# Kernel tuning notes

Measured on AMD Instinct MI355X. Metric: run time of the kernel, lower is better.

The kernel has to match this reference:

```python
import jax, jax.numpy as jnp
import numpy as np

N = 16384          # num nodes (128 graphs x 128 turbines)
E = 262144         # edges before self loops
TURBINE_NUM = 128
D_IN = 512         # input_dim (= 2*hidden_dim1)
H1 = 256           # hidden_dim1
H2 = 256           # hidden_dim2
NEG_SLOPE = 0.2    # PyG GATConv default leaky relu slope


def _glorot(key, shape, fan_in):
    return jax.random.normal(key, shape, dtype=jnp.float32) / np.sqrt(fan_in)


def setup_inputs() -> dict:
    key = jax.random.key(0)
    ks = jax.random.split(key, 12)
    x = jax.random.normal(ks[0], (N, H2), dtype=jnp.float32)
    adj = jax.random.randint(ks[1], (2, E), 0, N, dtype=jnp.int64)
    # fc: Linear(hidden_dim2 -> hidden_dim1); stored as [in, out]
    W_fc = _glorot(ks[2], (H2, H1), H2)
    b_fc = jnp.zeros((H1,), dtype=jnp.float32)
    # gat1: GATConv(H1 -> H1, heads=2, concat)
    W1 = _glorot(ks[3], (H1, 2 * H1), H1)
    a1_src = _glorot(ks[4], (2, H1), H1)
    a1_dst = _glorot(ks[5], (2, H1), H1)
    b1 = jnp.zeros((2 * H1,), dtype=jnp.float32)
    # gat2: GATConv(D_IN -> D_IN, heads=1, concat)
    W2 = _glorot(ks[6], (D_IN, D_IN), D_IN)
    a2_src = _glorot(ks[7], (1, D_IN), D_IN)
    a2_dst = _glorot(ks[8], (1, D_IN), D_IN)
    b2 = jnp.zeros((D_IN,), dtype=jnp.float32)
    return dict(x=x, adj=adj, W_fc=W_fc, b_fc=b_fc, W1=W1, a1_src=a1_src,
                a1_dst=a1_dst, b1=b1, W2=W2, a2_src=a2_src, a2_dst=a2_dst, b2=b2)


def gat_conv(x, src, dst, W, a_src, a_dst, bias, heads, out_ch):
    """PyG GATConv (eval mode, self loops already in src/dst)."""
    n = x.shape[0]
    h = (x @ W).reshape(n, heads, out_ch)                 # [N,H,C]
    al_s = jnp.einsum('nhc,hc->nh', h, a_src)             # [N,H]
    al_d = jnp.einsum('nhc,hc->nh', h, a_dst)
    e = jax.nn.leaky_relu(al_s[src] + al_d[dst], NEG_SLOPE)  # [E,H]
    # segment softmax over incoming edges per destination node
    e_max = jax.ops.segment_max(e, dst, num_segments=n)
    e_exp = jnp.exp(e - e_max[dst])
    denom = jax.ops.segment_sum(e_exp, dst, num_segments=n)
    alpha = e_exp / (denom[dst] + 1e-16)                  # [E,H]
    msg = h[src] * alpha[:, :, None]                      # [E,H,C]
    out = jax.ops.segment_sum(msg, dst, num_segments=n)   # [N,H,C]
    return out.reshape(n, heads * out_ch) + bias


def reference(x, adj, W_fc, b_fc, W1, a1_src, a1_dst, b1, W2, a2_src, a2_dst, b2):
    # add self loops (PyG GATConv default)
    loops = jnp.arange(N, dtype=adj.dtype)
    src = jnp.concatenate([adj[0], loops])
    dst = jnp.concatenate([adj[1], loops])
    h = jax.nn.relu(x @ W_fc + b_fc)                      # fc + ReLU
    h = gat_conv(h, src, dst, W1, a1_src, a1_dst, b1, heads=2, out_ch=H1)
    h = jax.nn.relu(h)
    h = gat_conv(h, src, dst, W2, a2_src, a2_dst, b2, heads=1, out_ch=D_IN)
    y = jax.nn.relu(h)
    return y.reshape(-1, TURBINE_NUM, y.shape[1])         # [128,128,512]
```

## Files before the change

### kernel.cpp

```cpp
#include <hip/hip_runtime.h>

#define N_NODES 16384
#define N_EDGES 262144
#define E_TOT   (N_EDGES + N_NODES)
#define NEG_SLOPE 0.2f
#define SLOTS 64

typedef __attribute__((ext_vector_type(8))) short short8;
typedef __attribute__((ext_vector_type(4))) float floatx4;
typedef __attribute__((ext_vector_type(4))) int intx4;

__device__ __forceinline__ float bf2f(ushort u) {
    return __uint_as_float(((unsigned)u) << 16);
}
__device__ __forceinline__ ushort f2bf(float f) {
    unsigned u = __float_as_uint(f);
    u += 0x7fffu + ((u >> 16) & 1u);
    return (ushort)(u >> 16);
}
__device__ __forceinline__ float leaky(float x) {
    return x > 0.f ? x : NEG_SLOPE * x;
}

#define PREP_T1     65536
#define PREP_T2     (PREP_T1 + 131072)
#define PREP_Z      (PREP_T2 + 262144)
#define PREP_ZA     (PREP_Z + 4096)
#define PREP_V      (PREP_ZA + 24576)
#define PREP_TOT    (PREP_V + 131072)

__global__ __launch_bounds__(256) void k_prep(const float* __restrict__ Wfc,
                                              ushort* __restrict__ WfcT,
                                              const float* __restrict__ W1,
                                              ushort* __restrict__ W1T,
                                              const float* __restrict__ W2,
                                              ushort* __restrict__ W2T,
                                              int* __restrict__ counts,
                                              int* __restrict__ alzero,
                                              const float* __restrict__ a1s,
                                              const float* __restrict__ a1d,
                                              const float* __restrict__ a2s,
                                              const float* __restrict__ a2d,
                                              float* __restrict__ v1s,
                                              float* __restrict__ v1d,
                                              float* __restrict__ v2s,
                                              float* __restrict__ v2d) {
    int idx = blockIdx.x * 256 + threadIdx.x;
    if (idx < PREP_T1) {
        int t = idx;
        int k = t >> 8, n = t & 255;
        WfcT[n * 256 + k] = f2bf(Wfc[t]);
    } else if (idx < PREP_T2) {
        int t = idx - PREP_T1;
        int k = t >> 9, n = t & 511;
        W1T[n * 256 + k] = f2bf(W1[t]);
    } else if (idx < PREP_Z) {
        int t = idx - PREP_T2;
        int k = t >> 9, n = t & 511;
        W2T[n * 512 + k] = f2bf(W2[t]);
    } else if (idx < PREP_ZA) {
        int t = idx - PREP_Z;
        *(intx4*)(counts + t * 4) = (intx4){0, 0, 0, 0};
    } else if (idx < PREP_V) {
        int t = idx - PREP_ZA;
        *(intx4*)(alzero + t * 4) = (intx4){0, 0, 0, 0};
    } else if (idx < PREP_TOT) {
        int t = idx - PREP_V;
        int w = t >> 6, lane = t & 63;
        int grp = w >> 9;
        int o = w & 511;
        float sum;
        if (grp < 2) {
            const float* a = grp ? a1d : a1s;
            int h = o >> 8, k = o & 255;
            const float* wr = W1 + (size_t)k * 512 + h * 256;
            const float* ar = a + h * 256;
            floatx4 wv = *(const floatx4*)(wr + lane * 4);
            floatx4 av = *(const floatx4*)(ar + lane * 4);
            sum = wv[0]*av[0] + wv[1]*av[1] + wv[2]*av[2] + wv[3]*av[3];
        } else {
            const float* a = (grp == 2) ? a2s : a2d;
            const float* wr = W2 + (size_t)o * 512;
            floatx4 w0 = *(const floatx4*)(wr + lane * 8);
            floatx4 w1 = *(const floatx4*)(wr + lane * 8 + 4);
            floatx4 a0 = *(const floatx4*)(a + lane * 8);
            floatx4 a1 = *(const floatx4*)(a + lane * 8 + 4);
            sum = w0[0]*a0[0] + w0[1]*a0[1] + w0[2]*a0[2] + w0[3]*a0[3]
                + w1[0]*a1[0] + w1[1]*a1[1] + w1[2]*a1[2] + w1[3]*a1[3];
        }
#pragma unroll
        for (int msk = 1; msk < 64; msk <<= 1) sum += __shfl_xor(sum, msk, 64);
        if (lane == 0) {
            float* dst = (grp == 0) ? v1s : (grp == 1) ? v1d
                        : (grp == 2) ? v2s : v2d;
            dst[o] = sum;
        }
    }
}

__global__ __launch_bounds__(256) void k_scatter(const int* __restrict__ adj,
                                                 int* __restrict__ counts,
                                                 int* __restrict__ esrc) {
    int e = blockIdx.x * 256 + threadIdx.x;
    if (e < E_TOT) {
        int s, d;
        if (e < N_EDGES) { s = adj[e]; d = adj[N_EDGES + e]; }
        else             { s = e - N_EDGES; d = s; }
        int pos = atomicAdd(&counts[d], 1);
        esrc[(d << 6) + pos] = s;
    }
}

#define GM 128
#define GN 128
#define GK 64
#define LDK2 72

__global__ __launch_bounds__(256) void gemm128(const void* __restrict__ Av,
                                               int a_f32, int lda, int agrp,
                                               const ushort* __restrict__ BT,
                                               const float* __restrict__ bias,
                                               ushort* __restrict__ C,
                                               float* __restrict__ Cf,
                                               int Nc, int K, int relu,
                                               const float* __restrict__ vs,
                                               const float* __restrict__ vd,
                                               float* __restrict__ als,
                                               float* __restrict__ ald,
                                               int heads) {
    __shared__ ushort As[GM * LDK2];
    __shared__ ushort Bs[GN * LDK2];
    int tid = threadIdx.x, wave = tid >> 6, lane = tid & 63;
    int quad = lane >> 4, l16 = lane & 15;
    int bm = blockIdx.x * GM, bn = blockIdx.y * GN;
    int wm = (wave & 1) * 64, wn = (wave >> 1) * 64;
    int abase = (bn >> 8) * agrp;

    const ushort* Ab = (const ushort*)Av;
    const float*  Af = (const float*)Av;

    floatx4 acc[4][4];
#pragma unroll
    for (int mi = 0; mi < 4; mi++)
#pragma unroll
        for (int ni = 0; ni < 4; ni++)
            acc[mi][ni] = (floatx4){0.f, 0.f, 0.f, 0.f};

    int srow[4], scol[4];
#pragma unroll
    for (int t = 0; t < 4; t++) {
        int ci = tid + 256 * t;
        srow[t] = ci >> 3;
        scol[t] = (ci & 7) * 8;
    }

    short8 av[4], bv[4];
    floatx4 fa0[4], fa1[4];

    if (a_f32) {
#pragma unroll
        for (int t = 0; t < 4; t++) {
            const float* pa = Af + (size_t)(bm + srow[t]) * lda + abase + scol[t];
            fa0[t] = *(const floatx4*)pa;
            fa1[t] = *(const floatx4*)(pa + 4);
        }
    } else {
#pragma unroll
        for (int t = 0; t < 4; t++)
            av[t] = *(const short8*)(Ab + (size_t)(bm + srow[t]) * lda + abase + scol[t]);
    }
#pragma unroll
    for (int t = 0; t < 4; t++)
        bv[t] = *(const short8*)(BT + (size_t)(bn + srow[t]) * K + scol[t]);

    for (int kb = 0; kb < K; kb += GK) {
        if (kb) {
            asm volatile("s_waitcnt lgkmcnt(0)" ::: "memory");
            __builtin_amdgcn_sched_barrier(0);
            __builtin_amdgcn_s_barrier();
            __builtin_amdgcn_sched_barrier(0);
        }
        if (a_f32) {
#pragma unroll
            for (int t = 0; t < 4; t++) {
                short8 r;
                r[0] = (short)f2bf(fa0[t][0]); r[1] = (short)f2bf(fa0[t][1]);
                r[2] = (short)f2bf(fa0[t][2]); r[3] = (short)f2bf(fa0[t][3]);
                r[4] = (short)f2bf(fa1[t][0]); r[5] = (short)f2bf(fa1[t][1]);
                r[6] = (short)f2bf(fa1[t][2]); r[7] = (short)f2bf(fa1[t][3]);
                *(short8*)&As[srow[t] * LDK2 + scol[t]] = r;
            }
        } else {
#pragma unroll
            for (int t = 0; t < 4; t++)
                *(short8*)&As[srow[t] * LDK2 + scol[t]] = av[t];
        }
#pragma unroll
        for (int t = 0; t < 4; t++)
            *(short8*)&Bs[srow[t] * LDK2 + scol[t]] = bv[t];
        asm volatile("s_waitcnt lgkmcnt(0)" ::: "memory");
        __builtin_amdgcn_sched_barrier(0);
        __builtin_amdgcn_s_barrier();
        __builtin_amdgcn_sched_barrier(0);

        if (kb + GK < K) {
            if (a_f32) {
#pragma unroll
                for (int t = 0; t < 4; t++) {
                    const float* pa = Af + (size_t)(bm + srow[t]) * lda + abase + kb + GK + scol[t];
                    fa0[t] = *(const floatx4*)pa;
                    fa1[t] = *(const floatx4*)(pa + 4);
                }
            } else {
#pragma unroll
                for (int t = 0; t < 4; t++)
                    av[t] = *(const short8*)(Ab + (size_t)(bm + srow[t]) * lda + abase + kb + GK + scol[t]);
            }
#pragma unroll
            for (int t = 0; t < 4; t++)
                bv[t] = *(const short8*)(BT + (size_t)(bn + srow[t]) * K + kb + GK + scol[t]);
            __builtin_amdgcn_sched_barrier(0);
        }

#pragma unroll
        for (int kk = 0; kk < GK; kk += 32) {
            short8 af[4], bf[4];
#pragma unroll
            for (int mi = 0; mi < 4; mi++)
                af[mi] = *(const short8*)&As[(wm + mi * 16 + l16) * LDK2 + kk + quad * 8];
#pragma unroll
            for (int ni = 0; ni < 4; ni++)
                bf[ni] = *(const short8*)&Bs[(wn + ni * 16 + l16) * LDK2 + kk + quad * 8];
#pragma unroll
            for (int mi = 0; mi < 4; mi++)
#pragma unroll
                for (int ni = 0; ni < 4; ni++)
                    acc[mi][ni] = __builtin_amdgcn_mfma_f32_16x16x32_bf16(
                        af[mi], bf[ni], acc[mi][ni], 0, 0, 0);
        }
    }

#pragma unroll
    for (int mi = 0; mi < 4; mi++) {
        int row = bm + wm + mi * 16 + quad * 4;
#pragma unroll
        for (int ni = 0; ni < 4; ni++) {
            int col = bn + wn + ni * 16 + l16;
            float bv2 = bias ? bias[col] : 0.f;
#pragma unroll
            for (int i = 0; i < 4; i++) {
                float v = acc[mi][ni][i] + bv2;
                if (relu) v = fmaxf(v, 0.f);
                acc[mi][ni][i] = v;
                if (Cf) Cf[(size_t)(row + i) * Nc + col] = v;
                else    C[(size_t)(row + i) * Nc + col] = f2bf(v);
            }
        }
    }

    if (als) {
        if (heads == 2) {
            float s0[4], s1[4], d0[4], d1[4];
#pragma unroll
            for (int ni = 0; ni < 4; ni++) {
                int col = bn + wn + ni * 16 + l16;
                s0[ni] = vs[col];  s1[ni] = vs[256 + col];
                d0[ni] = vd[col];  d1[ni] = vd[256 + col];
            }
#pragma unroll
            for (int mi = 0; mi < 4; mi++) {
#pragma unroll
                for (int i = 0; i < 4; i++) {
                    float aS0 = 0.f, aS1 = 0.f, aD0 = 0.f, aD1 = 0.f;
#pragma unroll
                    for (int ni = 0; ni < 4; ni++) {
                        float vv = acc[mi][ni][i];
                        aS0 += vv * s0[ni]; aS1 += vv * s1[ni];
                        aD0 += vv * d0[ni]; aD1 += vv * d1[ni];
                    }
#pragma unroll
                    for (int msk = 1; msk < 16; msk <<= 1) {
                        aS0 += __shfl_xor(aS0, msk, 64);
                        aS1 += __shfl_xor(aS1, msk, 64);
                        aD0 += __shfl_xor(aD0, msk, 64);
                        aD1 += __shfl_xor(aD1, msk, 64);
                    }
                    if (l16 == 0) {
                        int row = bm + wm + mi * 16 + quad * 4 + i;
                        atomicAdd(&als[row * 2],     aS0);
                        atomicAdd(&als[row * 2 + 1], aS1);
                        atomicAdd(&ald[row * 2],     aD0);
                        atomicAdd(&ald[row * 2 + 1], aD1);
                    }
                }
            }
        } else {
            float aS[4], aD[4];
#pragma unroll
            for (int ni = 0; ni < 4; ni++) {
                int col = bn + wn + ni * 16 + l16;
                aS[ni] = vs[col];
                aD[ni] = vd[col];
            }
#pragma unroll
            for (int mi = 0; mi < 4; mi++) {
#pragma unroll
                for (int i = 0; i < 4; i++) {
                    float dS = 0.f, dD = 0.f;
#pragma unroll
                    for (int ni = 0; ni < 4; ni++) {
                        dS += acc[mi][ni][i] * aS[ni];
                        dD += acc[mi][ni][i] * aD[ni];
                    }
#pragma unroll
                    for (int msk = 1; msk < 16; msk <<= 1) {
                        dS += __shfl_xor(dS, msk, 64);
                        dD += __shfl_xor(dD, msk, 64);
                    }
                    if (l16 == 0) {
                        int row = bm + wm + mi * 16 + quad * 4 + i;
                        atomicAdd(&als[row], dS);
                        atomicAdd(&ald[row], dD);
                    }
                }
            }
        }
    }
}

__global__ __launch_bounds__(256) void k_agg(const ushort* __restrict__ h,
                                             const float* __restrict__ als,
                                             const float* __restrict__ ald,
                                             const int* __restrict__ counts,
                                             const int* __restrict__ esrc,
                                             ushort* __restrict__ outb,
                                             int heads) {
    int wave = threadIdx.x >> 6, lane = threadIdx.x & 63;
    int n = blockIdx.x * 4 + wave;
    int base = n << 6;
    int deg  = counts[n];

    int myhead = (heads == 2) ? (lane >> 5) : 0;
    int cs = (heads == 2) ? ((lane & 31) * 8) : (lane * 8);
    int stride = (heads == 2) ? 256 : 512;

    float aldh0 = ald[n * heads];
    float aldh1 = (heads == 2) ? ald[n * heads + 1] : 0.f;
    const ushort* hc = h + cs;

    float acc[8];
#pragma unroll
    for (int q = 0; q < 8; q++) acc[q] = 0.f;
    float ws0 = 0.f, ws1 = 0.f;

    for (int cb = 0; cb < deg; cb += 64) {
        int i = cb + lane;
        int sv = 0;
        float w0 = 0.f, w1 = 0.f;
        if (i < deg) {
            sv = esrc[base + i];
            w0 = __expf(leaky(als[sv * heads] + aldh0));
            if (heads == 2) w1 = __expf(leaky(als[sv * 2 + 1] + aldh1));
            ws0 += w0; ws1 += w1;
        }
        int cnt = min(64, deg - cb);
        int j = 0;
        for (; j + 4 <= cnt; j += 4) {
            int sj0 = __shfl(sv, j, 64);
            int sj1 = __shfl(sv, j + 1, 64);
            int sj2 = __shfl(sv, j + 2, 64);
            int sj3 = __shfl(sv, j + 3, 64);
            float a00 = __shfl(w0, j, 64),     a01 = __shfl(w1, j, 64);
            float a10 = __shfl(w0, j + 1, 64), a11 = __shfl(w1, j + 1, 64);
            float a20 = __shfl(w0, j + 2, 64), a21 = __shfl(w1, j + 2, 64);
            float a30 = __shfl(w0, j + 3, 64), a31 = __shfl(w1, j + 3, 64);
            float al0 = myhead ? a01 : a00;
            float al1 = myhead ? a11 : a10;
            float al2 = myhead ? a21 : a20;
            float al3 = myhead ? a31 : a30;
            short8 h0v = *(const short8*)(hc + (size_t)sj0 * stride);
            short8 h1v = *(const short8*)(hc + (size_t)sj1 * stride);
            short8 h2v = *(const short8*)(hc + (size_t)sj2 * stride);
            short8 h3v = *(const short8*)(hc + (size_t)sj3 * stride);
#pragma unroll
            for (int q = 0; q < 8; q++) {
                acc[q] += al0 * bf2f((ushort)h0v[q]);
                acc[q] += al1 * bf2f((ushort)h1v[q]);
                acc[q] += al2 * bf2f((ushort)h2v[q]);
                acc[q] += al3 * bf2f((ushort)h3v[q]);
            }
        }
        for (; j < cnt; j++) {
            int s = __shfl(sv, j, 64);
            float a0 = __shfl(w0, j, 64), a1 = __shfl(w1, j, 64);
            float al = myhead ? a1 : a0;
            short8 hv = *(const short8*)(hc + (size_t)s * stride);
#pragma unroll
            for (int q = 0; q < 8; q++) acc[q] += al * bf2f((ushort)hv[q]);
        }
    }

#pragma unroll
    for (int msk = 1; msk < 64; msk <<= 1) {
        ws0 += __shfl_xor(ws0, msk, 64);
        ws1 += __shfl_xor(ws1, msk, 64);
    }
    float inv = 1.f / ((myhead ? ws1 : ws0) + 1e-16f);

    short8 r;
#pragma unroll
    for (int q = 0; q < 8; q++) r[q] = (short)f2bf(acc[q] * inv);
    *(short8*)(outb + (size_t)n * 512 + lane * 8) = r;
}

extern "C" void kernel_launch(void* const* d_in, const int* in_sizes, int n_in,
                              void* d_out, int out_size, void* d_ws, size_t ws_size,
                              hipStream_t stream) {
    const float* x   = (const float*)d_in[0];
    const int*   adj = (const int*)d_in[1];
    const float* Wfc = (const float*)d_in[2];
    const float* bfc = (const float*)d_in[3];
    const float* W1  = (const float*)d_in[4];
    const float* a1s = (const float*)d_in[5];
    const float* a1d = (const float*)d_in[6];
    const float* b1  = (const float*)d_in[7];
    const float* W2  = (const float*)d_in[8];
    const float* a2s = (const float*)d_in[9];
    const float* a2d = (const float*)d_in[10];
    const float* b2  = (const float*)d_in[11];
    float* out = (float*)d_out;

    char* ws = (char*)d_ws;
    size_t off = 0;
    auto alloc = [&](size_t bytes) -> void* {
        void* p = ws + off;
        off += (bytes + 255) & ~(size_t)255;
        return p;
    };
    ushort* h0b  = (ushort*)alloc((size_t)N_NODES * 256 * 2);
    ushort* hub  = (ushort*)alloc((size_t)N_NODES * 512 * 2);
    ushort* g1b  = (ushort*)alloc((size_t)N_NODES * 512 * 2);
    int* counts  = (int*)alloc(N_NODES * 4);
    int* esrc    = (int*)alloc((size_t)N_NODES * SLOTS * 4);
    ushort* WfcT = (ushort*)alloc(256 * 256 * 2);
    ushort* W1T  = (ushort*)alloc(512 * 256 * 2);
    ushort* W2T  = (ushort*)alloc(512 * 512 * 2);
    float* als1  = (float*)alloc(N_NODES * 2 * 4);
    float* ald1  = (float*)alloc(N_NODES * 2 * 4);
    float* als2  = (float*)alloc(N_NODES * 4);
    float* ald2  = (float*)alloc(N_NODES * 4);
    float* v1s   = (float*)alloc(512 * 4);
    float* v1d   = (float*)alloc(512 * 4);
    float* v2s   = (float*)alloc(512 * 4);
    float* v2d   = (float*)alloc(512 * 4);

    k_prep<<<PREP_TOT / 256, 256, 0, stream>>>(Wfc, WfcT, W1, W1T, W2, W2T,
                                               counts, (int*)als1,
                                               a1s, a1d, a2s, a2d,
                                               v1s, v1d, v2s, v2d);

    k_scatter<<<(E_TOT + 255) / 256, 256, 0, stream>>>(adj, counts, esrc);

    gemm128<<<dim3(N_NODES / GM, 256 / GN), 256, 0, stream>>>(
        x, 1, 256, 0, WfcT, bfc, h0b, nullptr, 256, 256, 1,
        v1s, v1d, als1, ald1, 2);
    k_agg<<<N_NODES / 4, 256, 0, stream>>>(h0b, als1, ald1, counts, esrc, hub, 2);

    gemm128<<<dim3(N_NODES / GM, 512 / GN), 256, 0, stream>>>(
        hub, 0, 512, 256, W1T, b1, g1b, nullptr, 512, 256, 1,
        v2s, v2d, als2, ald2, 1);
    k_agg<<<N_NODES / 4, 256, 0, stream>>>(g1b, als2, ald2, counts, esrc, hub, 1);

    gemm128<<<dim3(N_NODES / GM, 512 / GN), 256, 0, stream>>>(
        hub, 0, 512, 0, W2T, b2, nullptr, out, 512, 512, 1,
        nullptr, nullptr, nullptr, nullptr, 0);
}
```

Measured before the change: 220.7 us.

## Split GEMM into LDS fp32-input kernel and direct-register bf16 GEMM without shared memory

The generic GEMM is split into two kernels. One is a specialized LDS-staged kernel for the first fp32-input layer with compile-time dimensions. The other, a new gemm_direct used for the bf16 layers, loads MFMA fragments straight from global memory into registers with double-buffered prefetch, skipping the LDS stage and its barriers. This removes LDS writes and sync overhead, but each wave now reads A and B tiles redundantly from global/L2 (no sharing across waves), and the loads are short strided 16-byte rows that may coalesce less well.

```diff
diff --git a/kernel.cpp b/kernel.cpp
--- a/kernel.cpp
+++ b/kernel.cpp
@@ -116,28 +116,21 @@
 #define GK 64
 #define LDK2 72
 
-__global__ __launch_bounds__(256) void gemm128(const void* __restrict__ Av,
-                                               int a_f32, int lda, int agrp,
-                                               const ushort* __restrict__ BT,
-                                               const float* __restrict__ bias,
-                                               ushort* __restrict__ C,
-                                               float* __restrict__ Cf,
-                                               int Nc, int K, int relu,
-                                               const float* __restrict__ vs,
-                                               const float* __restrict__ vd,
-                                               float* __restrict__ als,
-                                               float* __restrict__ ald,
-                                               int heads) {
+__global__ __launch_bounds__(256) void gemm1_lds(const float* __restrict__ Af,
+                                                 const ushort* __restrict__ BT,
+                                                 const float* __restrict__ bias,
+                                                 ushort* __restrict__ C,
+                                                 const float* __restrict__ vs,
+                                                 const float* __restrict__ vd,
+                                                 float* __restrict__ als,
+                                                 float* __restrict__ ald) {
     __shared__ ushort As[GM * LDK2];
     __shared__ ushort Bs[GN * LDK2];
+    const int lda = 256, K = 256, Nc = 256;
     int tid = threadIdx.x, wave = tid >> 6, lane = tid & 63;
     int quad = lane >> 4, l16 = lane & 15;
     int bm = blockIdx.x * GM, bn = blockIdx.y * GN;
     int wm = (wave & 1) * 64, wn = (wave >> 1) * 64;
-    int abase = (bn >> 8) * agrp;
-
-    const ushort* Ab = (const ushort*)Av;
-    const float*  Af = (const float*)Av;
 
     floatx4 acc[4][4];
 #pragma unroll
@@ -154,24 +147,15 @@
         scol[t] = (ci & 7) * 8;
     }
 
-    short8 av[4], bv[4];
+    short8 bv[4];
     floatx4 fa0[4], fa1[4];
-
-    if (a_f32) {
-#pragma unroll
-        for (int t = 0; t < 4; t++) {
-            const float* pa = Af + (size_t)(bm + srow[t]) * lda + abase + scol[t];
-            fa0[t] = *(const floatx4*)pa;
-            fa1[t] = *(const floatx4*)(pa + 4);
-        }
-    } else {
-#pragma unroll
-        for (int t = 0; t < 4; t++)
-            av[t] = *(const short8*)(Ab + (size_t)(bm + srow[t]) * lda + abase + scol[t]);
-    }
-#pragma unroll
-    for (int t = 0; t < 4; t++)
+#pragma unroll
+    for (int t = 0; t < 4; t++) {
+        const float* pa = Af + (size_t)(bm + srow[t]) * lda + scol[t];
+        fa0[t] = *(const floatx4*)pa;
+        fa1[t] = *(const floatx4*)(pa + 4);
         bv[t] = *(const short8*)(BT + (size_t)(bn + srow[t]) * K + scol[t]);
+    }
 
     for (int kb = 0; kb < K; kb += GK) {
         if (kb) {
@@ -180,45 +164,29 @@
             __builtin_amdgcn_s_barrier();
             __builtin_amdgcn_sched_barrier(0);
         }
-        if (a_f32) {
-#pragma unroll
-            for (int t = 0; t < 4; t++) {
-                short8 r;
-                r[0] = (short)f2bf(fa0[t][0]); r[1] = (short)f2bf(fa0[t][1]);
-                r[2] = (short)f2bf(fa0[t][2]); r[3] = (short)f2bf(fa0[t][3]);
-                r[4] = (short)f2bf(fa1[t][0]); r[5] = (short)f2bf(fa1[t][1]);
-                r[6] = (short)f2bf(fa1[t][2]); r[7] = (short)f2bf(fa1[t][3]);
-                *(short8*)&As[srow[t] * LDK2 + scol[t]] = r;
-            }
-        } else {
-#pragma unroll
-            for (int t = 0; t < 4; t++)
-                *(short8*)&As[srow[t] * LDK2 + scol[t]] = av[t];
-        }
-#pragma unroll
-        for (int t = 0; t < 4; t++)
+#pragma unroll
+        for (int t = 0; t < 4; t++) {
+            short8 r;
+            r[0] = (short)f2bf(fa0[t][0]); r[1] = (short)f2bf(fa0[t][1]);
+            r[2] = (short)f2bf(fa0[t][2]); r[3] = (short)f2bf(fa0[t][3]);
+            r[4] = (short)f2bf(fa1[t][0]); r[5] = (short)f2bf(fa1[t][1]);
+            r[6] = (short)f2bf(fa1[t][2]); r[7] = (short)f2bf(fa1[t][3]);
+            *(short8*)&As[srow[t] * LDK2 + scol[t]] = r;
             *(short8*)&Bs[srow[t] * LDK2 + scol[t]] = bv[t];
+        }
         asm volatile("s_waitcnt lgkmcnt(0)" ::: "memory");
         __builtin_amdgcn_sched_barrier(0);
         __builtin_amdgcn_s_barrier();
         __builtin_amdgcn_sched_barrier(0);
 
         if (kb + GK < K) {
-            if (a_f32) {
-#pragma unroll
-                for (int t = 0; t < 4; t++) {
-                    const float* pa = Af + (size_t)(bm + srow[t]) * lda + abase + kb + GK + scol[t];
-                    fa0[t] = *(const floatx4*)pa;
-                    fa1[t] = *(const floatx4*)(pa + 4);
-                }
-            } else {
-#pragma unroll
-                for (int t = 0; t < 4; t++)
-                    av[t] = *(const short8*)(Ab + (size_t)(bm + srow[t]) * lda + abase + kb + GK + scol[t]);
-            }
-#pragma unroll
-            for (int t = 0; t < 4; t++)
+#pragma unroll
+            for (int t = 0; t < 4; t++) {
+                const float* pa = Af + (size_t)(bm + srow[t]) * lda + kb + GK + scol[t];
+                fa0[t] = *(const floatx4*)pa;
+                fa1[t] = *(const floatx4*)(pa + 4);
                 bv[t] = *(const short8*)(BT + (size_t)(bn + srow[t]) * K + kb + GK + scol[t]);
+            }
             __builtin_amdgcn_sched_barrier(0);
         }
 
@@ -237,6 +205,128 @@
                 for (int ni = 0; ni < 4; ni++)
                     acc[mi][ni] = __builtin_amdgcn_mfma_f32_16x16x32_bf16(
                         af[mi], bf[ni], acc[mi][ni], 0, 0, 0);
+        }
+    }
+
+#pragma unroll
+    for (int mi = 0; mi < 4; mi++) {
+        int row = bm + wm + mi * 16 + quad * 4;
+#pragma unroll
+        for (int ni = 0; ni < 4; ni++) {
+            int col = bn + wn + ni * 16 + l16;
+            float bv2 = bias[col];
+#pragma unroll
+            for (int i = 0; i < 4; i++) {
+                float v = fmaxf(acc[mi][ni][i] + bv2, 0.f);
+                acc[mi][ni][i] = v;
+                C[(size_t)(row + i) * Nc + col] = f2bf(v);
+            }
+        }
+    }
+
+    float s0[4], s1[4], d0[4], d1[4];
+#pragma unroll
+    for (int ni = 0; ni < 4; ni++) {
+        int col = bn + wn + ni * 16 + l16;
+        s0[ni] = vs[col];  s1[ni] = vs[256 + col];
+        d0[ni] = vd[col];  d1[ni] = vd[256 + col];
+    }
+#pragma unroll
+    for (int mi = 0; mi < 4; mi++) {
+#pragma unroll
+        for (int i = 0; i < 4; i++) {
+            float aS0 = 0.f, aS1 = 0.f, aD0 = 0.f, aD1 = 0.f;
+#pragma unroll
+            for (int ni = 0; ni < 4; ni++) {
+                float vv = acc[mi][ni][i];
+                aS0 += vv * s0[ni]; aS1 += vv * s1[ni];
+                aD0 += vv * d0[ni]; aD1 += vv * d1[ni];
+            }
+#pragma unroll
+            for (int msk = 1; msk < 16; msk <<= 1) {
+                aS0 += __shfl_xor(aS0, msk, 64);
+                aS1 += __shfl_xor(aS1, msk, 64);
+                aD0 += __shfl_xor(aD0, msk, 64);
+                aD1 += __shfl_xor(aD1, msk, 64);
+            }
+            if (l16 == 0) {
+                int row = bm + wm + mi * 16 + quad * 4 + i;
+                atomicAdd(&als[row * 2],     aS0);
+                atomicAdd(&als[row * 2 + 1], aS1);
+                atomicAdd(&ald[row * 2],     aD0);
+                atomicAdd(&ald[row * 2 + 1], aD1);
+            }
+        }
+    }
+}
+
+__global__ __launch_bounds__(256) void gemm_direct(const ushort* __restrict__ A,
+                                                   int lda, int agrp,
+                                                   const ushort* __restrict__ BT,
+                                                   const float* __restrict__ bias,
+                                                   ushort* __restrict__ C,
+                                                   float* __restrict__ Cf,
+                                                   int Nc, int K, int relu,
+                                                   const float* __restrict__ vs,
+                                                   const float* __restrict__ vd,
+                                                   float* __restrict__ als,
+                                                   float* __restrict__ ald) {
+    int tid = threadIdx.x, wave = tid >> 6, lane = tid & 63;
+    int quad = lane >> 4, l16 = lane & 15;
+    int bm = blockIdx.x * GM, bn = blockIdx.y * GN;
+    int wm = (wave & 1) * 64, wn = (wave >> 1) * 64;
+    int abase = (bn >> 8) * agrp;
+
+    const ushort* Ap[4];
+    const ushort* Bp[4];
+#pragma unroll
+    for (int mi = 0; mi < 4; mi++)
+        Ap[mi] = A + (size_t)(bm + wm + mi * 16 + l16) * lda + abase + quad * 8;
+#pragma unroll
+    for (int ni = 0; ni < 4; ni++)
+        Bp[ni] = BT + (size_t)(bn + wn + ni * 16 + l16) * K + quad * 8;
+
+    floatx4 acc[4][4];
+#pragma unroll
+    for (int mi = 0; mi < 4; mi++)
+#pragma unroll
+        for (int ni = 0; ni < 4; ni++)
+            acc[mi][ni] = (floatx4){0.f, 0.f, 0.f, 0.f};
+
+    short8 a0[4], b0[4], a1[4], b1[4];
+#pragma unroll
+    for (int mi = 0; mi < 4; mi++) a0[mi] = *(const short8*)(Ap[mi]);
+#pragma unroll
+    for (int ni = 0; ni < 4; ni++) b0[ni] = *(const short8*)(Bp[ni]);
+#pragma unroll
+    for (int mi = 0; mi < 4; mi++) a1[mi] = *(const short8*)(Ap[mi] + 32);
+#pragma unroll
+    for (int ni = 0; ni < 4; ni++) b1[ni] = *(const short8*)(Bp[ni] + 32);
+
+    for (int kk = 0; kk < K; kk += 64) {
+#pragma unroll
+        for (int mi = 0; mi < 4; mi++)
+#pragma unroll
+            for (int ni = 0; ni < 4; ni++)
+                acc[mi][ni] = __builtin_amdgcn_mfma_f32_16x16x32_bf16(
+                    a0[mi], b0[ni], acc[mi][ni], 0, 0, 0);
+        if (kk + 64 < K) {
+#pragma unroll
+            for (int mi = 0; mi < 4; mi++) a0[mi] = *(const short8*)(Ap[mi] + kk + 64);
+#pragma unroll
+            for (int ni = 0; ni < 4; ni++) b0[ni] = *(const short8*)(Bp[ni] + kk + 64);
+        }
+#pragma unroll
+        for (int mi = 0; mi < 4; mi++)
+#pragma unroll
+            for (int ni = 0; ni < 4; ni++)
+                acc[mi][ni] = __builtin_amdgcn_mfma_f32_16x16x32_bf16(
+                    a1[mi], b1[ni], acc[mi][ni], 0, 0, 0);
+        if (kk + 96 < K) {
+#pragma unroll
+            for (int mi = 0; mi < 4; mi++) a1[mi] = *(const short8*)(Ap[mi] + kk + 96);
+#pragma unroll
+            for (int ni = 0; ni < 4; ni++) b1[ni] = *(const short8*)(Bp[ni] + kk + 96);
         }
     }
 
@@ -259,69 +349,32 @@
     }
 
     if (als) {
-        if (heads == 2) {
-            float s0[4], s1[4], d0[4], d1[4];
-#pragma unroll
-            for (int ni = 0; ni < 4; ni++) {
-                int col = bn + wn + ni * 16 + l16;
-                s0[ni] = vs[col];  s1[ni] = vs[256 + col];
-                d0[ni] = vd[col];  d1[ni] = vd[256 + col];
-            }
-#pragma unroll
-            for (int mi = 0; mi < 4; mi++) {
-#pragma unroll
-                for (int i = 0; i < 4; i++) {
-                    float aS0 = 0.f, aS1 = 0.f, aD0 = 0.f, aD1 = 0.f;
-#pragma unroll
-                    for (int ni = 0; ni < 4; ni++) {
-                        float vv = acc[mi][ni][i];
-                        aS0 += vv * s0[ni]; aS1 += vv * s1[ni];
-                        aD0 += vv * d0[ni]; aD1 += vv * d1[ni];
-                    }
-#pragma unroll
-                    for (int msk = 1; msk < 16; msk <<= 1) {
-                        aS0 += __shfl_xor(aS0, msk, 64);
-                        aS1 += __shfl_xor(aS1, msk, 64);
-                        aD0 += __shfl_xor(aD0, msk, 64);
-                        aD1 += __shfl_xor(aD1, msk, 64);
-                    }
-                    if (l16 == 0) {
-                        int row = bm + wm + mi * 16 + quad * 4 + i;
-                        atomicAdd(&als[row * 2],     aS0);
-                        atomicAdd(&als[row * 2 + 1], aS1);
-                        atomicAdd(&ald[row * 2],     aD0);
-                        atomicAdd(&ald[row * 2 + 1], aD1);
-                    }
+        float aS[4], aD[4];
+#pragma unroll
+        for (int ni = 0; ni < 4; ni++) {
+            int col = bn + wn + ni * 16 + l16;
+            aS[ni] = vs[col];
+            aD[ni] = vd[col];
+        }
+#pragma unroll
+        for (int mi = 0; mi < 4; mi++) {
+#pragma unroll
+            for (int i = 0; i < 4; i++) {
+                float dS = 0.f, dD = 0.f;
+#pragma unroll
+                for (int ni = 0; ni < 4; ni++) {
+                    dS += acc[mi][ni][i] * aS[ni];
+                    dD += acc[mi][ni][i] * aD[ni];
                 }
-            }
-        } else {
-            float aS[4], aD[4];
-#pragma unroll
-            for (int ni = 0; ni < 4; ni++) {
-                int col = bn + wn + ni * 16 + l16;
-                aS[ni] = vs[col];
-                aD[ni] = vd[col];
-            }
-#pragma unroll
-            for (int mi = 0; mi < 4; mi++) {
-#pragma unroll
-                for (int i = 0; i < 4; i++) {
-                    float dS = 0.f, dD = 0.f;
-#pragma unroll
-                    for (int ni = 0; ni < 4; ni++) {
-                        dS += acc[mi][ni][i] * aS[ni];
-                        dD += acc[mi][ni][i] * aD[ni];
-                    }
-#pragma unroll
-                    for (int msk = 1; msk < 16; msk <<= 1) {
-                        dS += __shfl_xor(dS, msk, 64);
-                        dD += __shfl_xor(dD, msk, 64);
-                    }
-                    if (l16 == 0) {
-                        int row = bm + wm + mi * 16 + quad * 4 + i;
-                        atomicAdd(&als[row], dS);
-                        atomicAdd(&ald[row], dD);
-                    }
+#pragma unroll
+                for (int msk = 1; msk < 16; msk <<= 1) {
+                    dS += __shfl_xor(dS, msk, 64);
+                    dD += __shfl_xor(dD, msk, 64);
+                }
+                if (l16 == 0) {
+                    int row = bm + wm + mi * 16 + quad * 4 + i;
+                    atomicAdd(&als[row], dS);
+                    atomicAdd(&ald[row], dD);
                 }
             }
         }
@@ -461,17 +514,16 @@
 
     k_scatter<<<(E_TOT + 255) / 256, 256, 0, stream>>>(adj, counts, esrc);
 
-    gemm128<<<dim3(N_NODES / GM, 256 / GN), 256, 0, stream>>>(
-        x, 1, 256, 0, WfcT, bfc, h0b, nullptr, 256, 256, 1,
-        v1s, v1d, als1, ald1, 2);
+    gemm1_lds<<<dim3(N_NODES / GM, 256 / GN), 256, 0, stream>>>(
+        x, WfcT, bfc, h0b, v1s, v1d, als1, ald1);
     k_agg<<<N_NODES / 4, 256, 0, stream>>>(h0b, als1, ald1, counts, esrc, hub, 2);
 
-    gemm128<<<dim3(N_NODES / GM, 512 / GN), 256, 0, stream>>>(
-        hub, 0, 512, 256, W1T, b1, g1b, nullptr, 512, 256, 1,
-        v2s, v2d, als2, ald2, 1);
+    gemm_direct<<<dim3(N_NODES / GM, 512 / GN), 256, 0, stream>>>(
+        hub, 512, 256, W1T, b1, g1b, nullptr, 512, 256, 1,
+        v2s, v2d, als2, ald2);
     k_agg<<<N_NODES / 4, 256, 0, stream>>>(g1b, als2, ald2, counts, esrc, hub, 1);
 
-    gemm128<<<dim3(N_NODES / GM, 512 / GN), 256, 0, stream>>>(
-        hub, 0, 512, 0, W2T, b2, nullptr, out, 512, 512, 1,
-        nullptr, nullptr, nullptr, nullptr, 0);
-}
+    gemm_direct<<<dim3(N_NODES / GM, 512 / GN), 256, 0, stream>>>(
+        hub, 512, 0, W2T, b2, nullptr, out, 512, 512, 1,
+        nullptr, nullptr, nullptr, nullptr);
+}
```

After: 242.4 us. +9.8%, slower.

## Split K across two wave groups per GEMM block with LDS reduction

Applied to the files above, without the earlier changes.

Each GEMM block now runs 512 threads, with two groups of four waves each computing half of the K dimension into separate LDS tiles. Partial accumulators from the second group are written to shared memory and summed by the first group before the epilogue. This aims to add more waves per CU and hide latency for a small grid of tiles. In exchange it adds an LDS reduction, extra barriers and higher LDS use per block, which may limit occupancy.

```diff
diff --git a/kernel.cpp b/kernel.cpp
--- a/kernel.cpp
+++ b/kernel.cpp
@@ -116,25 +116,29 @@
 #define GK 64
 #define LDK2 72
 
-__global__ __launch_bounds__(256) void gemm128(const void* __restrict__ Av,
-                                               int a_f32, int lda, int agrp,
-                                               const ushort* __restrict__ BT,
-                                               const float* __restrict__ bias,
-                                               ushort* __restrict__ C,
-                                               float* __restrict__ Cf,
-                                               int Nc, int K, int relu,
-                                               const float* __restrict__ vs,
-                                               const float* __restrict__ vd,
-                                               float* __restrict__ als,
-                                               float* __restrict__ ald,
-                                               int heads) {
-    __shared__ ushort As[GM * LDK2];
-    __shared__ ushort Bs[GN * LDK2];
+__global__ __launch_bounds__(512, 4) void gemm128_sk(const void* __restrict__ Av,
+                                                     int a_f32, int lda, int agrp,
+                                                     const ushort* __restrict__ BT,
+                                                     const float* __restrict__ bias,
+                                                     ushort* __restrict__ C,
+                                                     float* __restrict__ Cf,
+                                                     int Nc, int K, int relu,
+                                                     const float* __restrict__ vs,
+                                                     const float* __restrict__ vd,
+                                                     float* __restrict__ als,
+                                                     float* __restrict__ ald,
+                                                     int heads) {
+    __shared__ ushort Sh[2 * (GM + GN) * LDK2];
     int tid = threadIdx.x, wave = tid >> 6, lane = tid & 63;
+    int kw = wave >> 2, wsub = wave & 3;
     int quad = lane >> 4, l16 = lane & 15;
     int bm = blockIdx.x * GM, bn = blockIdx.y * GN;
-    int wm = (wave & 1) * 64, wn = (wave >> 1) * 64;
+    int wm = (wsub & 1) * 64, wn = (wsub >> 1) * 64;
     int abase = (bn >> 8) * agrp;
+    int K2 = K >> 1;
+    int kofs = kw * K2;
+    ushort* As = Sh + kw * (GM * LDK2);
+    ushort* Bs = Sh + 2 * GM * LDK2 + kw * (GN * LDK2);
 
     const ushort* Ab = (const ushort*)Av;
     const float*  Af = (const float*)Av;
@@ -146,10 +150,11 @@
         for (int ni = 0; ni < 4; ni++)
             acc[mi][ni] = (floatx4){0.f, 0.f, 0.f, 0.f};
 
+    int tid2 = tid & 255;
     int srow[4], scol[4];
 #pragma unroll
     for (int t = 0; t < 4; t++) {
-        int ci = tid + 256 * t;
+        int ci = tid2 + 256 * t;
         srow[t] = ci >> 3;
         scol[t] = (ci & 7) * 8;
     }
@@ -160,20 +165,20 @@
     if (a_f32) {
 #pragma unroll
         for (int t = 0; t < 4; t++) {
-            const float* pa = Af + (size_t)(bm + srow[t]) * lda + abase + scol[t];
+            const float* pa = Af + (size_t)(bm + srow[t]) * lda + abase + kofs + scol[t];
             fa0[t] = *(const floatx4*)pa;
             fa1[t] = *(const floatx4*)(pa + 4);
         }
     } else {
 #pragma unroll
         for (int t = 0; t < 4; t++)
-            av[t] = *(const short8*)(Ab + (size_t)(bm + srow[t]) * lda + abase + scol[t]);
+            av[t] = *(const short8*)(Ab + (size_t)(bm + srow[t]) * lda + abase + kofs + scol[t]);
     }
 #pragma unroll
     for (int t = 0; t < 4; t++)
-        bv[t] = *(const short8*)(BT + (size_t)(bn + srow[t]) * K + scol[t]);
-
-    for (int kb = 0; kb < K; kb += GK) {
+        bv[t] = *(const short8*)(BT + (size_t)(bn + srow[t]) * K + kofs + scol[t]);
+
+    for (int kb = 0; kb < K2; kb += GK) {
         if (kb) {
             asm volatile("s_waitcnt lgkmcnt(0)" ::: "memory");
             __builtin_amdgcn_sched_barrier(0);
@@ -203,22 +208,22 @@
         __builtin_amdgcn_s_barrier();
         __builtin_amdgcn_sched_barrier(0);
 
-        if (kb + GK < K) {
+        if (kb + GK < K2) {
             if (a_f32) {
 #pragma unroll
                 for (int t = 0; t < 4; t++) {
-                    const float* pa = Af + (size_t)(bm + srow[t]) * lda + abase + kb + GK + scol[t];
+                    const float* pa = Af + (size_t)(bm + srow[t]) * lda + abase + kofs + kb + GK + scol[t];
                     fa0[t] = *(const floatx4*)pa;
                     fa1[t] = *(const floatx4*)(pa + 4);
                 }
             } else {
 #pragma unroll
                 for (int t = 0; t < 4; t++)
-                    av[t] = *(const short8*)(Ab + (size_t)(bm + srow[t]) * lda + abase + kb + GK + scol[t]);
+                    av[t] = *(const short8*)(Ab + (size_t)(bm + srow[t]) * lda + abase + kofs + kb + GK + scol[t]);
             }
 #pragma unroll
             for (int t = 0; t < 4; t++)
-                bv[t] = *(const short8*)(BT + (size_t)(bn + srow[t]) * K + kb + GK + scol[t]);
+                bv[t] = *(const short8*)(BT + (size_t)(bn + srow[t]) * K + kofs + kb + GK + scol[t]);
             __builtin_amdgcn_sched_barrier(0);
         }
 
@@ -239,6 +244,35 @@
                         af[mi], bf[ni], acc[mi][ni], 0, 0, 0);
         }
     }
+
+    asm volatile("s_waitcnt lgkmcnt(0)" ::: "memory");
+    __builtin_amdgcn_sched_barrier(0);
+    __builtin_amdgcn_s_barrier();
+    __builtin_amdgcn_sched_barrier(0);
+
+    float* comb = (float*)Sh;
+    if (kw == 1) {
+#pragma unroll
+        for (int mi = 0; mi < 4; mi++)
+#pragma unroll
+            for (int ni = 0; ni < 4; ni++)
+#pragma unroll
+                for (int i = 0; i < 4; i++)
+                    comb[((wsub * 64) + (mi * 16 + ni * 4 + i)) * 64 + lane] = acc[mi][ni][i];
+    }
+    asm volatile("s_waitcnt lgkmcnt(0)" ::: "memory");
+    __builtin_amdgcn_sched_barrier(0);
+    __builtin_amdgcn_s_barrier();
+    __builtin_amdgcn_sched_barrier(0);
+    if (kw == 1) return;
+
+#pragma unroll
+    for (int mi = 0; mi < 4; mi++)
+#pragma unroll
+        for (int ni = 0; ni < 4; ni++)
+#pragma unroll
+            for (int i = 0; i < 4; i++)
+                acc[mi][ni][i] += comb[((wsub * 64) + (mi * 16 + ni * 4 + i)) * 64 + lane];
 
 #pragma unroll
     for (int mi = 0; mi < 4; mi++) {
@@ -461,17 +495,17 @@
 
     k_scatter<<<(E_TOT + 255) / 256, 256, 0, stream>>>(adj, counts, esrc);
 
-    gemm128<<<dim3(N_NODES / GM, 256 / GN), 256, 0, stream>>>(
+    gemm128_sk<<<dim3(N_NODES / GM, 256 / GN), 512, 0, stream>>>(
         x, 1, 256, 0, WfcT, bfc, h0b, nullptr, 256, 256, 1,
         v1s, v1d, als1, ald1, 2);
     k_agg<<<N_NODES / 4, 256, 0, stream>>>(h0b, als1, ald1, counts, esrc, hub, 2);
 
-    gemm128<<<dim3(N_NODES / GM, 512 / GN), 256, 0, stream>>>(
+    gemm128_sk<<<dim3(N_NODES / GM, 512 / GN), 512, 0, stream>>>(
         hub, 0, 512, 256, W1T, b1, g1b, nullptr, 512, 256, 1,
         v2s, v2d, als2, ald2, 1);
     k_agg<<<N_NODES / 4, 256, 0, stream>>>(g1b, als2, ald2, counts, esrc, hub, 1);
 
-    gemm128<<<dim3(N_NODES / GM, 512 / GN), 256, 0, stream>>>(
+    gemm128_sk<<<dim3(N_NODES / GM, 512 / GN), 512, 0, stream>>>(
         hub, 0, 512, 0, W2T, b2, nullptr, out, 512, 512, 1,
         nullptr, nullptr, nullptr, nullptr, 0);
 }
```

After: 360.3 us. 1.63x slower.
